# Kernel optimization log

Measured on AMD Instinct MI355X. Metric: run time of the kernel, lower is better.

Reference implementation:

```python
import jax, jax.numpy as jnp
import numpy as np

RADIUS = 8
STRIDE = 4
EPS = 1e-5
B, N, C, O = 4, 16384, 64, 64
S = 2 * RADIUS


def _bn(x, gamma, beta, mean, var):
    # inference-mode BatchNorm1d
    return (x - mean) / jnp.sqrt(var + EPS) * gamma + beta


def _circular_grouping_index(batch, n_points):
    # neighbors at circular offsets -radius..-1, 1..radius along the point sequence
    offsets = jnp.concatenate([jnp.arange(-RADIUS, 0), jnp.arange(1, RADIUS + 1)])  # (S,)
    idx = (jnp.arange(n_points)[:, None] + offsets[None, :]) % n_points             # (N,S)
    gidx = jnp.arange(batch)[:, None, None] * n_points + idx[None]                  # (B,N,S)
    return gidx.reshape(-1)


def setup_inputs() -> dict:
    key = jax.random.key(0)
    ks = jax.random.split(key, 8)
    inp = {
        "points": jax.random.normal(ks[0], (B, N, 2), dtype=jnp.float32),
        "features": jax.random.normal(ks[1], (B * N, C), dtype=jnp.float32),
        # modules_1: Linear(2+C -> C, no bias), BN(C), ReLU, Linear(C -> 1)
        "w1": jax.random.normal(ks[2], (2 + C, C), dtype=jnp.float32) * 0.05,
        "bn1_gamma": jnp.ones((C,), jnp.float32),
        "bn1_beta": jnp.zeros((C,), jnp.float32),
        "bn1_mean": jnp.zeros((C,), jnp.float32),
        "bn1_var": jnp.ones((C,), jnp.float32),
        "w2": jax.random.normal(ks[3], (C, 1), dtype=jnp.float32) * 0.05,
        "b2": jnp.zeros((1,), jnp.float32),
        # modules_2: Linear(C -> O, no bias), BN(O), ReLU
        "w3": jax.random.normal(ks[4], (C, O), dtype=jnp.float32) * 0.05,
        "bn2_gamma": jnp.ones((O,), jnp.float32),
        "bn2_beta": jnp.zeros((O,), jnp.float32),
        "bn2_mean": jnp.zeros((O,), jnp.float32),
        "bn2_var": jnp.ones((O,), jnp.float32),
    }
    return inp


def reference(points, features, w1, bn1_gamma, bn1_beta, bn1_mean, bn1_var,
              w2, b2, w3, bn2_gamma, bn2_beta, bn2_mean, bn2_var):
    batch, n_points, _ = points.shape
    gidx = _circular_grouping_index(batch, n_points)                 # (B*N*S,)

    nn_points = points.reshape(-1, 2)[gidx].reshape(batch, n_points, S, 2)
    translation = (nn_points - points[:, :, None])[:, ::STRIDE].reshape(-1, 2)

    nn_features = features[gidx].reshape(batch, n_points, S, -1)     # (B,N,S,C)
    nn_feat_str = nn_features[:, ::STRIDE].reshape(-1, features.shape[1])

    # attention weights
    h = jnp.concatenate([translation, nn_feat_str], axis=1) @ w1
    h = jax.nn.relu(_bn(h, bn1_gamma, bn1_beta, bn1_mean, bn1_var))
    w = h @ w2 + b2                                                  # (-1,1)
    w = jax.nn.softmax(w.reshape(-1, S, 1), axis=1)

    # value branch (computed on all gathered rows, then strided, as in original)
    y = jax.nn.relu(_bn(features[gidx] @ w3, bn2_gamma, bn2_beta, bn2_mean, bn2_var))
    y = y.reshape(batch, n_points, S, -1)[:, ::STRIDE].reshape(-1, S, O)

    outputs = jnp.sum(y * w, axis=1)                                 # (B*N/stride, O)
    points_out = points[:, ::STRIDE]
    return points_out, outputs
```

## Files before the change

kernel.cpp:

```cpp
#include <hip/hip_runtime.h>
#include <hip/hip_bf16.h>

#define NPTS   16384
#define NMASK  16383
#define EPSV   1e-5f
#define OUTOFF 32768

typedef __attribute__((ext_vector_type(8))) short short8_t;
typedef __attribute__((ext_vector_type(4))) short short4_t;
typedef __attribute__((ext_vector_type(4))) float f32x4;

static __device__ __forceinline__ short f2bf(float x) {
    union { __hip_bfloat16 b; short s; } u; u.b = __float2bfloat16(x); return u.s;
}
static __device__ __forceinline__ float bf2f(short s) {
    union { float f; unsigned u; } v; v.u = ((unsigned)(unsigned short)s) << 16; return v.f;
}

__global__ __launch_bounds__(256, 2) void fused_std_kernel(
    const float* __restrict__ points,
    const float* __restrict__ features,
    const float* __restrict__ w1,
    const float* __restrict__ bn1_gamma, const float* __restrict__ bn1_beta,
    const float* __restrict__ bn1_mean,  const float* __restrict__ bn1_var,
    const float* __restrict__ w2,
    const float* __restrict__ w3,
    const float* __restrict__ bn2_gamma, const float* __restrict__ bn2_beta,
    const float* __restrict__ bn2_mean,  const float* __restrict__ bn2_var,
    float* __restrict__ d_out)
{
    __shared__ __align__(16) short wlds[8192];
    __shared__ __align__(16) short gpls[160 * 64];
    __shared__ __align__(16) short ylds[160 * 64];
    __shared__ __align__(16) float ptsl[160 * 2];
    __shared__ float cP[64], cQ[64], cW2[64], cS1[64], cB1[64], cS2[64], cB2[64];
    __shared__ __align__(16) float swp[4][16];

    const int tid = threadIdx.x;
    const int wv  = tid >> 6, l = tid & 63;
    const int r   = l & 15,  kg = l >> 4;
    const int bi  = blockIdx.x >> 7;
    const int n0  = (blockIdx.x & 127) * 128;
    const int base = bi * NPTS;

    struct TF { float4 a, b, c, d; };
    auto loadTile = [&](int ti) {
        const int gr = base + ((n0 - 16 + ti * 16 + r) & NMASK);
        const float* fp = features + (size_t)gr * 64 + kg * 8;
        TF t;
        t.a = *(const float4*)(fp);
        t.b = *(const float4*)(fp + 4);
        t.c = *(const float4*)(fp + 32);
        t.d = *(const float4*)(fp + 36);
        return t;
    };
    TF T0 = loadTile(wv);
    TF T1 = loadTile(wv + 4);
    TF T2;
    if (wv < 2) T2 = loadTile(wv + 8);

    for (int e = tid; e < 8192; e += 256) {
        const int mat = e >> 12, idx = e & 4095;
        const int k = idx >> 6, col = idx & 63;
        const float v = mat ? w3[idx] : w1[idx + 128];
        const int byte = mat * 8192 + col * 128 + ((k * 2) ^ ((col & 7) << 4));
        *(short*)((char*)wlds + byte) = f2bf(v);
    }
    if (tid < 64) {
        const float s1 = bn1_gamma[tid] * rsqrtf(bn1_var[tid] + EPSV);
        cS1[tid] = s1;
        cB1[tid] = bn1_beta[tid] - bn1_mean[tid] * s1;
        cP[tid]  = s1 * w1[tid];
        cQ[tid]  = s1 * w1[64 + tid];
        cW2[tid] = w2[tid];
        const float s2 = bn2_gamma[tid] * rsqrtf(bn2_var[tid] + EPSV);
        cS2[tid] = s2;
        cB2[tid] = bn2_beta[tid] - bn2_mean[tid] * s2;
    }
    for (int t = tid; t < 160; t += 256) {
        const int gr = base + ((n0 - 16 + t) & NMASK);
        *(float2*)&ptsl[t * 2] = *(const float2*)&points[(size_t)gr * 2];
    }
    __syncthreads();

    auto processTile = [&](const TF& t, int ti) {
        short8_t f0, f1;
        f0[0]=f2bf(t.a.x); f0[1]=f2bf(t.a.y); f0[2]=f2bf(t.a.z); f0[3]=f2bf(t.a.w);
        f0[4]=f2bf(t.b.x); f0[5]=f2bf(t.b.y); f0[6]=f2bf(t.b.z); f0[7]=f2bf(t.b.w);
        f1[0]=f2bf(t.c.x); f1[1]=f2bf(t.c.y); f1[2]=f2bf(t.c.z); f1[3]=f2bf(t.c.w);
        f1[4]=f2bf(t.d.x); f1[5]=f2bf(t.d.y); f1[6]=f2bf(t.d.z); f1[7]=f2bf(t.d.w);
        const f32x4 z = {0.f, 0.f, 0.f, 0.f};
        f32x4 acc0[4] = {z, z, z, z}, acc1[4] = {z, z, z, z};
        #pragma unroll
        for (int tt = 0; tt < 4; ++tt) {
            const int col = 16 * tt + r;
            #pragma unroll
            for (int s = 0; s < 2; ++s) {
                const int wb = col * 128 + ((s * 64 + kg * 16) ^ ((r & 7) << 4));
                const short8_t wa = *(const short8_t*)((const char*)wlds + wb);
                acc0[tt] = __builtin_amdgcn_mfma_f32_16x16x32_bf16(wa, s ? f1 : f0, acc0[tt], 0, 0, 0);
                const short8_t wb3 = *(const short8_t*)((const char*)wlds + 8192 + wb);
                acc1[tt] = __builtin_amdgcn_mfma_f32_16x16x32_bf16(wb3, s ? f1 : f0, acc1[tt], 0, 0, 0);
            }
        }
        const int row = ti * 16 + r;
        #pragma unroll
        for (int tt = 0; tt < 4; ++tt) {
            const int c0 = 16 * tt + kg * 4;
            short4_t gq, yq;
            #pragma unroll
            for (int j = 0; j < 4; ++j) {
                gq[j] = f2bf(fmaf(acc0[tt][j], cS1[c0 + j], cB1[c0 + j]));
                yq[j] = f2bf(fmaxf(fmaf(acc1[tt][j], cS2[c0 + j], cB2[c0 + j]), 0.0f));
            }
            const int byte = row * 128 +
                (((2 * tt + (kg >> 1)) ^ (row & 7)) << 4) + ((kg & 1) << 3);
            *(short4_t*)((char*)gpls + byte) = gq;
            *(short4_t*)((char*)ylds + byte) = yq;
        }
    };
    processTile(T0, wv);
    processTile(T1, wv + 4);
    if (wv < 2) processTile(T2, wv + 8);
    __syncthreads();

    const int knb  = r;
    const int cgrp = kg;
    const int offk = (knb < 8) ? knb - 8 : knb - 7;
    float P0[8], P1[8], Q0[8], Q1[8];
    #pragma unroll
    for (int e = 0; e < 8; ++e) {
        P0[e] = cP[cgrp * 8 + e];  P1[e] = cP[32 + cgrp * 8 + e];
        Q0[e] = cQ[cgrp * 8 + e];  Q1[e] = cQ[32 + cgrp * 8 + e];
    }
    short8_t Bw0, Bw1;
    #pragma unroll
    for (int e = 0; e < 8; ++e) {
        Bw0[e] = f2bf(knb == 0 ? cW2[cgrp * 8 + e] : 0.0f);
        Bw1[e] = f2bf(knb == 0 ? cW2[32 + cgrp * 8 + e] : 0.0f);
    }

    for (int p = wv; p < 32; p += 4) {
        const int crow = 16 + 4 * p;
        const int nrow = crow + offk;
        const float tx = ptsl[nrow * 2]     - ptsl[crow * 2];
        const float ty = ptsl[nrow * 2 + 1] - ptsl[crow * 2 + 1];
        const short8_t g0 = *(const short8_t*)((const char*)gpls +
            nrow * 128 + ((cgrp ^ (nrow & 7)) << 4));
        const short8_t g1 = *(const short8_t*)((const char*)gpls +
            nrow * 128 + (((4 + cgrp) ^ (nrow & 7)) << 4));
        short8_t A0, A1;
        #pragma unroll
        for (int e = 0; e < 8; ++e) {
            const float a0 = bf2f(g0[e]) + tx * P0[e] + ty * Q0[e];
            A0[e] = f2bf(fmaxf(a0, 0.0f));
            const float a1 = bf2f(g1[e]) + tx * P1[e] + ty * Q1[e];
            A1[e] = f2bf(fmaxf(a1, 0.0f));
        }
        f32x4 D = {0.f, 0.f, 0.f, 0.f};
        D = __builtin_amdgcn_mfma_f32_16x16x32_bf16(A0, Bw0, D, 0, 0, 0);
        D = __builtin_amdgcn_mfma_f32_16x16x32_bf16(A1, Bw1, D, 0, 0, 0);
        if (knb == 0) *(f32x4*)&swp[wv][cgrp * 4] = D;
        asm volatile("s_waitcnt lgkmcnt(0)" ::: "memory");
        float sc[16];
        #pragma unroll
        for (int q = 0; q < 4; ++q) {
            const f32x4 sv = *(const f32x4*)&swp[wv][q * 4];
            sc[q*4+0] = sv[0]; sc[q*4+1] = sv[1]; sc[q*4+2] = sv[2]; sc[q*4+3] = sv[3];
        }
        float mx = sc[0];
        #pragma unroll
        for (int k = 1; k < 16; ++k) mx = fmaxf(mx, sc[k]);
        float se = 0.0f, o = 0.0f;
        #pragma unroll
        for (int k = 0; k < 16; ++k) {
            const float ek = __expf(sc[k] - mx);
            se += ek;
            const int rk = crow + ((k < 8) ? k - 8 : k - 7);
            const short yb = *(const short*)((const char*)ylds +
                rk * 128 + ((((l >> 3) ^ (rk & 7))) << 4) + ((l & 7) << 1));
            o = fmaf(ek, bf2f(yb), o);
        }
        o /= se;
        const int pl = (n0 >> 2) + p;
        d_out[OUTOFF + ((size_t)bi * 4096 + pl) * 64 + l] = o;
        if (l < 2)
            d_out[((size_t)bi * 4096 + pl) * 2 + l] = ptsl[crow * 2 + l];
    }
}

extern "C" void kernel_launch(void* const* d_in, const int* in_sizes, int n_in,
                              void* d_out, int out_size, void* d_ws, size_t ws_size,
                              hipStream_t stream)
{
    const float* points    = (const float*)d_in[0];
    const float* features  = (const float*)d_in[1];
    const float* w1        = (const float*)d_in[2];
    const float* bn1_gamma = (const float*)d_in[3];
    const float* bn1_beta  = (const float*)d_in[4];
    const float* bn1_mean  = (const float*)d_in[5];
    const float* bn1_var   = (const float*)d_in[6];
    const float* w2        = (const float*)d_in[7];
    const float* w3        = (const float*)d_in[9];
    const float* bn2_gamma = (const float*)d_in[10];
    const float* bn2_beta  = (const float*)d_in[11];
    const float* bn2_mean  = (const float*)d_in[12];
    const float* bn2_var   = (const float*)d_in[13];

    fused_std_kernel<<<512, 256, 0, stream>>>(
        points, features, w1, bn1_gamma, bn1_beta, bn1_mean, bn1_var,
        w2, w3, bn2_gamma, bn2_beta, bn2_mean, bn2_var, (float*)d_out);
}
```

Before: 22.64 us.

## Halve block tile, share one LDS buffer for both projections, replace score MFMA with dot

```diff
diff --git a/kernel.cpp b/kernel.cpp
--- a/kernel.cpp
+++ b/kernel.cpp
@@ -17,7 +17,7 @@
     union { float f; unsigned u; } v; v.u = ((unsigned)(unsigned short)s) << 16; return v.f;
 }
 
-__global__ __launch_bounds__(256, 2) void fused_std_kernel(
+__global__ __launch_bounds__(256, 4) void fused_std_kernel(
     const float* __restrict__ points,
     const float* __restrict__ features,
     const float* __restrict__ w1,
@@ -30,17 +30,16 @@
     float* __restrict__ d_out)
 {
     __shared__ __align__(16) short wlds[8192];
-    __shared__ __align__(16) short gpls[160 * 64];
-    __shared__ __align__(16) short ylds[160 * 64];
-    __shared__ __align__(16) float ptsl[160 * 2];
+    __shared__ __align__(16) short xlds[96 * 64];
+    __shared__ __align__(16) float ptsl[96 * 2];
     __shared__ float cP[64], cQ[64], cW2[64], cS1[64], cB1[64], cS2[64], cB2[64];
-    __shared__ __align__(16) float swp[4][16];
+    __shared__ __align__(16) float ebuf[16][16];
 
     const int tid = threadIdx.x;
     const int wv  = tid >> 6, l = tid & 63;
     const int r   = l & 15,  kg = l >> 4;
-    const int bi  = blockIdx.x >> 7;
-    const int n0  = (blockIdx.x & 127) * 128;
+    const int bi  = blockIdx.x >> 8;
+    const int n0  = (blockIdx.x & 255) * 64;
     const int base = bi * NPTS;
 
     struct TF { float4 a, b, c, d; };
@@ -54,10 +53,9 @@
         t.d = *(const float4*)(fp + 36);
         return t;
     };
-    TF T0 = loadTile(wv);
-    TF T1 = loadTile(wv + 4);
-    TF T2;
-    if (wv < 2) T2 = loadTile(wv + 8);
+    TF Ta = loadTile(wv);
+    TF Tb;
+    if (wv < 2) Tb = loadTile(4 + wv);
 
     for (int e = tid; e < 8192; e += 256) {
         const int mat = e >> 12, idx = e & 4095;
@@ -77,13 +75,13 @@
         cS2[tid] = s2;
         cB2[tid] = bn2_beta[tid] - bn2_mean[tid] * s2;
     }
-    for (int t = tid; t < 160; t += 256) {
+    for (int t = tid; t < 96; t += 256) {
         const int gr = base + ((n0 - 16 + t) & NMASK);
         *(float2*)&ptsl[t * 2] = *(const float2*)&points[(size_t)gr * 2];
     }
     __syncthreads();
 
-    auto processTile = [&](const TF& t, int ti) {
+    auto mfma_tile = [&](const TF& t, int ti, short4_t* yc) {
         short8_t f0, f1;
         f0[0]=f2bf(t.a.x); f0[1]=f2bf(t.a.y); f0[2]=f2bf(t.a.z); f0[3]=f2bf(t.a.w);
         f0[4]=f2bf(t.b.x); f0[5]=f2bf(t.b.y); f0[6]=f2bf(t.b.z); f0[7]=f2bf(t.b.w);
@@ -99,8 +97,8 @@
                 const int wb = col * 128 + ((s * 64 + kg * 16) ^ ((r & 7) << 4));
                 const short8_t wa = *(const short8_t*)((const char*)wlds + wb);
                 acc0[tt] = __builtin_amdgcn_mfma_f32_16x16x32_bf16(wa, s ? f1 : f0, acc0[tt], 0, 0, 0);
-                const short8_t wb3 = *(const short8_t*)((const char*)wlds + 8192 + wb);
-                acc1[tt] = __builtin_amdgcn_mfma_f32_16x16x32_bf16(wb3, s ? f1 : f0, acc1[tt], 0, 0, 0);
+                const short8_t wc = *(const short8_t*)((const char*)wlds + 8192 + wb);
+                acc1[tt] = __builtin_amdgcn_mfma_f32_16x16x32_bf16(wc, s ? f1 : f0, acc1[tt], 0, 0, 0);
             }
         }
         const int row = ti * 16 + r;
@@ -115,74 +113,95 @@
             }
             const int byte = row * 128 +
                 (((2 * tt + (kg >> 1)) ^ (row & 7)) << 4) + ((kg & 1) << 3);
-            *(short4_t*)((char*)gpls + byte) = gq;
-            *(short4_t*)((char*)ylds + byte) = yq;
+            *(short4_t*)((char*)xlds + byte) = gq;
+            yc[tt] = yq;
         }
     };
-    processTile(T0, wv);
-    processTile(T1, wv + 4);
-    if (wv < 2) processTile(T2, wv + 8);
-    __syncthreads();
-
-    const int knb  = r;
-    const int cgrp = kg;
-    const int offk = (knb < 8) ? knb - 8 : knb - 7;
-    float P0[8], P1[8], Q0[8], Q1[8];
-    #pragma unroll
-    for (int e = 0; e < 8; ++e) {
-        P0[e] = cP[cgrp * 8 + e];  P1[e] = cP[32 + cgrp * 8 + e];
-        Q0[e] = cQ[cgrp * 8 + e];  Q1[e] = cQ[32 + cgrp * 8 + e];
-    }
-    short8_t Bw0, Bw1;
-    #pragma unroll
-    for (int e = 0; e < 8; ++e) {
-        Bw0[e] = f2bf(knb == 0 ? cW2[cgrp * 8 + e] : 0.0f);
-        Bw1[e] = f2bf(knb == 0 ? cW2[32 + cgrp * 8 + e] : 0.0f);
-    }
-
-    for (int p = wv; p < 32; p += 4) {
+    short4_t yA[4], yB[4];
+    mfma_tile(Ta, wv, yA);
+    if (wv < 2) mfma_tile(Tb, 4 + wv, yB);
+    __syncthreads();
+
+    const int offk = (r < 8) ? r - 8 : r - 7;
+    const f32x4 P0a = *(const f32x4*)&cP[kg * 8],      P0b = *(const f32x4*)&cP[kg * 8 + 4];
+    const f32x4 P1a = *(const f32x4*)&cP[32 + kg * 8], P1b = *(const f32x4*)&cP[32 + kg * 8 + 4];
+    const f32x4 Q0a = *(const f32x4*)&cQ[kg * 8],      Q0b = *(const f32x4*)&cQ[kg * 8 + 4];
+    const f32x4 Q1a = *(const f32x4*)&cQ[32 + kg * 8], Q1b = *(const f32x4*)&cQ[32 + kg * 8 + 4];
+    const f32x4 Wa  = *(const f32x4*)&cW2[kg * 8],     Wb  = *(const f32x4*)&cW2[kg * 8 + 4];
+    const f32x4 Wc  = *(const f32x4*)&cW2[32 + kg * 8],Wd  = *(const f32x4*)&cW2[32 + kg * 8 + 4];
+
+    #pragma unroll 1
+    for (int i = 0; i < 4; ++i) {
+        const int p = wv * 4 + i;
         const int crow = 16 + 4 * p;
         const int nrow = crow + offk;
-        const float tx = ptsl[nrow * 2]     - ptsl[crow * 2];
-        const float ty = ptsl[nrow * 2 + 1] - ptsl[crow * 2 + 1];
-        const short8_t g0 = *(const short8_t*)((const char*)gpls +
-            nrow * 128 + ((cgrp ^ (nrow & 7)) << 4));
-        const short8_t g1 = *(const short8_t*)((const char*)gpls +
-            nrow * 128 + (((4 + cgrp) ^ (nrow & 7)) << 4));
-        short8_t A0, A1;
-        #pragma unroll
-        for (int e = 0; e < 8; ++e) {
-            const float a0 = bf2f(g0[e]) + tx * P0[e] + ty * Q0[e];
-            A0[e] = f2bf(fmaxf(a0, 0.0f));
-            const float a1 = bf2f(g1[e]) + tx * P1[e] + ty * Q1[e];
-            A1[e] = f2bf(fmaxf(a1, 0.0f));
-        }
-        f32x4 D = {0.f, 0.f, 0.f, 0.f};
-        D = __builtin_amdgcn_mfma_f32_16x16x32_bf16(A0, Bw0, D, 0, 0, 0);
-        D = __builtin_amdgcn_mfma_f32_16x16x32_bf16(A1, Bw1, D, 0, 0, 0);
-        if (knb == 0) *(f32x4*)&swp[wv][cgrp * 4] = D;
-        asm volatile("s_waitcnt lgkmcnt(0)" ::: "memory");
-        float sc[16];
-        #pragma unroll
-        for (int q = 0; q < 4; ++q) {
-            const f32x4 sv = *(const f32x4*)&swp[wv][q * 4];
-            sc[q*4+0] = sv[0]; sc[q*4+1] = sv[1]; sc[q*4+2] = sv[2]; sc[q*4+3] = sv[3];
-        }
-        float mx = sc[0];
-        #pragma unroll
-        for (int k = 1; k < 16; ++k) mx = fmaxf(mx, sc[k]);
+        const float2 cpt = *(const float2*)&ptsl[crow * 2];
+        const float2 npt = *(const float2*)&ptsl[nrow * 2];
+        const float tx = npt.x - cpt.x, ty = npt.y - cpt.y;
+        const short8_t g0 = *(const short8_t*)((const char*)xlds +
+            nrow * 128 + ((kg ^ (nrow & 7)) << 4));
+        const short8_t g1 = *(const short8_t*)((const char*)xlds +
+            nrow * 128 + (((4 + kg) ^ (nrow & 7)) << 4));
+        float s = 0.0f;
+        #pragma unroll
+        for (int e = 0; e < 4; ++e) {
+            s = fmaf(fmaxf(bf2f(g0[e])     + tx * P0a[e] + ty * Q0a[e], 0.f), Wa[e], s);
+            s = fmaf(fmaxf(bf2f(g0[e + 4]) + tx * P0b[e] + ty * Q0b[e], 0.f), Wb[e], s);
+            s = fmaf(fmaxf(bf2f(g1[e])     + tx * P1a[e] + ty * Q1a[e], 0.f), Wc[e], s);
+            s = fmaf(fmaxf(bf2f(g1[e + 4]) + tx * P1b[e] + ty * Q1b[e], 0.f), Wd[e], s);
+        }
+        s += __shfl_xor(s, 16);
+        s += __shfl_xor(s, 32);
+        if (l < 16) ebuf[p][l] = s;
+    }
+    __syncthreads();
+
+    {
+        const int rowA = wv * 16 + r;
+        #pragma unroll
+        for (int tt = 0; tt < 4; ++tt) {
+            const int byte = rowA * 128 +
+                (((2 * tt + (kg >> 1)) ^ (rowA & 7)) << 4) + ((kg & 1) << 3);
+            *(short4_t*)((char*)xlds + byte) = yA[tt];
+        }
+        if (wv < 2) {
+            const int rowB = (4 + wv) * 16 + r;
+            #pragma unroll
+            for (int tt = 0; tt < 4; ++tt) {
+                const int byte = rowB * 128 +
+                    (((2 * tt + (kg >> 1)) ^ (rowB & 7)) << 4) + ((kg & 1) << 3);
+                *(short4_t*)((char*)xlds + byte) = yB[tt];
+            }
+        }
+    }
+    __syncthreads();
+
+    #pragma unroll 1
+    for (int i = 0; i < 4; ++i) {
+        const int p = wv * 4 + i;
+        const int crow = 16 + 4 * p;
+        const f32x4 sA = *(const f32x4*)&ebuf[p][0];
+        const f32x4 sB = *(const f32x4*)&ebuf[p][4];
+        const f32x4 sC = *(const f32x4*)&ebuf[p][8];
+        const f32x4 sD = *(const f32x4*)&ebuf[p][12];
+        float mx = fmaxf(fmaxf(fmaxf(sA[0], sA[1]), fmaxf(sA[2], sA[3])),
+                   fmaxf(fmaxf(sB[0], sB[1]), fmaxf(sB[2], sB[3])));
+        mx = fmaxf(mx, fmaxf(fmaxf(fmaxf(sC[0], sC[1]), fmaxf(sC[2], sC[3])),
+                              fmaxf(fmaxf(sD[0], sD[1]), fmaxf(sD[2], sD[3]))));
         float se = 0.0f, o = 0.0f;
         #pragma unroll
         for (int k = 0; k < 16; ++k) {
-            const float ek = __expf(sc[k] - mx);
+            const float sck = (k < 4) ? sA[k] : (k < 8) ? sB[k - 4]
+                             : (k < 12) ? sC[k - 8] : sD[k - 12];
+            const float ek = __expf(sck - mx);
             se += ek;
             const int rk = crow + ((k < 8) ? k - 8 : k - 7);
-            const short yb = *(const short*)((const char*)ylds +
-                rk * 128 + ((((l >> 3) ^ (rk & 7))) << 4) + ((l & 7) << 1));
+            const short yb = *(const short*)((const char*)xlds +
+                rk * 128 + (((l >> 3) ^ (rk & 7)) << 4) + ((l & 7) << 1));
             o = fmaf(ek, bf2f(yb), o);
         }
         o /= se;
-        const int pl = (n0 >> 2) + p;
+        const int pl = ((blockIdx.x & 255) << 4) + p;
         d_out[OUTOFF + ((size_t)bi * 4096 + pl) * 64 + l] = o;
         if (l < 2)
             d_out[((size_t)bi * 4096 + pl) * 2 + l] = ptsl[crow * 2 + l];
@@ -207,7 +226,7 @@
     const float* bn2_mean  = (const float*)d_in[12];
     const float* bn2_var   = (const float*)d_in[13];
 
-    fused_std_kernel<<<512, 256, 0, stream>>>(
+    fused_std_kernel<<<1024, 256, 0, stream>>>(
         points, features, w1, bn1_gamma, bn1_beta, bn1_mean, bn1_var,
         w2, w3, bn2_gamma, bn2_beta, bn2_mean, bn2_var, (float*)d_out);
 }
```

Measured after the change: 35.60 us. +57.2%, slower.
